# Kernel optimization log

Measured on AMD Instinct MI355X. Metric: run time of the kernel, lower is better.

## Reference

```python
import jax, jax.numpy as jnp
import numpy as np
from jax import lax

N, CIN, H, W = 128, 1024, 14, 14
CF, TH = 128, 128          # cv_filter, te_hidden
HP, GT, FP, A = 256, 256, 256, 32


def setup_inputs() -> dict:
    key = jax.random.key(0)
    ks = jax.random.split(key, 12)
    s = 0.05
    return {
        "image": jax.random.normal(ks[0], (N, CIN, H, W), jnp.float32),
        "code": jax.random.normal(ks[1], (N, TH), jnp.float32),
        "conv_w": jax.random.normal(ks[2], (CF, CIN, 3, 3), jnp.float32) * 0.02,
        "conv_b": jnp.zeros((CF,), jnp.float32),
        "hp_w0": jax.random.normal(ks[3], (CF + 2 + TH, HP), jnp.float32) * s,
        "hp_b0": jnp.zeros((HP,), jnp.float32),
        "hp_w1": jax.random.normal(ks[4], (HP, 1), jnp.float32) * s,
        "hp_b1": jnp.zeros((1,), jnp.float32),
        "gt_w0": jax.random.normal(ks[5], ((CF + 2) * 2 + TH, GT), jnp.float32) * s,
        "gt_b0": jnp.zeros((GT,), jnp.float32),
        "gt_w1": jax.random.normal(ks[6], (GT, GT), jnp.float32) * s,
        "gt_b1": jnp.zeros((GT,), jnp.float32),
        "fp_w0": jax.random.normal(ks[7], (GT, FP), jnp.float32) * s,
        "fp_b0": jnp.zeros((FP,), jnp.float32),
        "fp_w1": jax.random.normal(ks[8], (FP, A), jnp.float32) * s,
        "fp_b1": jnp.zeros((A,), jnp.float32),
    }


def _sarn(image, code, conv_w, conv_b, hp_w0, hp_b0, hp_w1, hp_b1,
          gt_w0, gt_b0, gt_w1, gt_b1, fp_w0, fp_b0, fp_w1, fp_b1):
    # visual_resize: 3x3 conv, stride 1, pad 1 (NCHW)
    x = lax.conv_general_dilated(image, conv_w, (1, 1), "SAME",
                                 dimension_numbers=("NCHW", "OIHW", "NCHW"))
    x = x + conv_b[None, :, None, None]                       # [n, cf, h, w]
    n, c, h, w = x.shape
    o = h * w
    # sarn_encode: append x/y coordinate channels and question code
    xc = jnp.broadcast_to(jnp.linspace(-1.0, 1.0, h).reshape(1, 1, h, 1), (n, 1, h, w))
    yc = jnp.broadcast_to(jnp.linspace(-1.0, 1.0, w).reshape(1, 1, 1, w), (n, 1, h, w))
    coord = jnp.concatenate([x, xc, yc], axis=1)              # [n, cf+2, h, w]
    q = jnp.broadcast_to(code[:, :, None, None], (n, code.shape[1], h, w))
    qenc = jnp.concatenate([coord, q], axis=1)                # [n, cf+2+th, h, w]
    ce = coord.reshape(n, c + 2, o).transpose(0, 2, 1)        # [n, o, cf+2]
    qe = qenc.reshape(n, -1, o).transpose(0, 2, 1)            # [n, o, cf+2+th]
    # h_psi: per-object attention logit
    a = jax.nn.relu(jnp.einsum("nod,dh->noh", qe, hp_w0) + hp_b0)
    att = jnp.einsum("noh,hk->nok", a, hp_w1) + hp_b1         # [n, o, 1]
    # sarn_pair: softmax select a single soft object, pair with every object
    sel = jax.nn.softmax(att[..., 0], axis=1)                 # [n, o]
    selected = jnp.einsum("no,nod->nd", sel, ce)              # [n, cf+2]
    pairs = jnp.concatenate(
        [qe, jnp.broadcast_to(selected[:, None, :], ce.shape)], axis=2)  # [n, o, 2*(cf+2)+th]
    # g_theta MLP + sum over objects
    g = jax.nn.relu(jnp.einsum("nop,pg->nog", pairs, gt_w0) + gt_b0)
    g = jax.nn.relu(jnp.einsum("nog,gk->nok", g, gt_w1) + gt_b1)
    relations = g.sum(axis=1)                                 # [n, gt]
    # f_phi MLP -> answer logits
    f = jax.nn.relu(relations @ fp_w0 + fp_b0)
    return f @ fp_w1 + fp_b1                                  # [n, a_size]


def reference(image, code, conv_w, conv_b, hp_w0, hp_b0, hp_w1, hp_b1,
              gt_w0, gt_b0, gt_w1, gt_b1, fp_w0, fp_b0, fp_w1, fp_b1):
    return _sarn(image, code, conv_w, conv_b, hp_w0, hp_b0, hp_w1, hp_b1,
                 gt_w0, gt_b0, gt_w1, gt_b1, fp_w0, fp_b0, fp_w1, fp_b1)
```

## Files before the change

kernel.cpp:

```cpp
#include <hip/hip_runtime.h>
#include <stdint.h>

typedef unsigned short u16;
typedef __bf16 bf16x8 __attribute__((ext_vector_type(8)));
typedef float f32x4 __attribute__((ext_vector_type(4)));

__device__ __forceinline__ u16 f2b(float f) {
  union { float f; uint32_t u; } v; v.f = f;
  uint32_t r = v.u + 0x7fffu + ((v.u >> 16) & 1u);
  return (u16)(r >> 16);
}
__device__ __forceinline__ float b2f(u16 b) {
  union { float f; uint32_t u; } v; v.u = ((uint32_t)b) << 16;
  return v.f;
}
__device__ __forceinline__ void g2l16(const void* g, void* l) {
  __builtin_amdgcn_global_load_lds(
      (const __attribute__((address_space(1))) void*)g,
      (__attribute__((address_space(3))) void*)l, 16, 0, 0);
}

#define N_SAMP 128
#define OPAD   224
#define ROWS   (N_SAMP * OPAD)
#define KQ     160

#define R_HP   40960
#define R_GT0  40960
#define R_GT1  65536
#define R_BHP  32768
#define R_BGT  32768
#define R_QC   (ROWS * 8)
#define R_QP   114688
#define R_ATT  7168
#define R_REL  8192
#define R_CNT  32
#define R_CVA  917504
__global__ __launch_bounds__(256) void prep_all(
    const float* __restrict__ conv_w, const float* __restrict__ image,
    const float* __restrict__ hp_w0, const float* __restrict__ gt_w0,
    const float* __restrict__ gt_w1, const float* __restrict__ hp_b0,
    const float* __restrict__ gt_b0, const float* __restrict__ code,
    u16* __restrict__ W2, u16* __restrict__ imgT,
    u16* __restrict__ hp_w0t, u16* __restrict__ gt_w0t, u16* __restrict__ gt_w1t,
    float* __restrict__ biasHP, float* __restrict__ biasGT, u16* __restrict__ qeb,
    float* __restrict__ att, float* __restrict__ relations,
    int* __restrict__ doneCnt, float* __restrict__ convAcc) {
  __shared__ float ls[64 * 197];
  int bid = blockIdx.x;
  int t = threadIdx.x;

  if (bid < 512) {
    int p0 = bid << 8;
    const float* src = conv_w + (size_t)p0 * 9;
#pragma unroll
    for (int i = 0; i < 9; ++i) ls[t + i * 256] = src[t + i * 256];
    __syncthreads();
#pragma unroll
    for (int s = 0; s < 9; ++s)
      W2[s * 131072 + p0 + t] = f2b(ls[t * 9 + s]);
    return;
  }
  bid -= 512;

  if (bid < 2048) {
    float (*tt)[197] = (float(*)[197])ls;
    int n = bid >> 4;
    int cin0 = (bid & 15) * 64;
    const float* src = image + ((size_t)n * 1024 + cin0) * 196;
    for (int e = t; e < 64 * 196; e += 256) {
      int c = e / 196, sp = e % 196;
      tt[c][sp] = src[c * 196 + sp];
    }
    __syncthreads();
#pragma unroll
    for (int i = 0; i < 8; ++i) {
      int qid = t + i * 256;
      int spg = qid >> 3, qd = qid & 7;
      int gy = spg >> 4, gx = spg & 15;
      uint4 pk = {0u, 0u, 0u, 0u};
      if (gy >= 1 && gy <= 14 && gx >= 1 && gx <= 14) {
        int sp = (gy - 1) * 14 + (gx - 1);
        uint32_t vv[8];
#pragma unroll
        for (int j = 0; j < 8; ++j) vv[j] = f2b(tt[qd * 8 + j][sp]);
        pk.x = vv[0] | (vv[1] << 16);
        pk.y = vv[2] | (vv[3] << 16);
        pk.z = vv[4] | (vv[5] << 16);
        pk.w = vv[6] | (vv[7] << 16);
      }
      *(uint4*)(imgT + (((size_t)(n * 256 + spg)) << 10) + cin0 + qd * 8) = pk;
    }
    return;
  }
  bid -= 2048;

  int idx = bid * 256 + t;
  if (idx < R_HP) {
    int nn = idx / KQ, kk = idx % KQ;
    hp_w0t[idx] = (kk < 130) ? f2b(hp_w0[kk * 256 + nn]) : (u16)0;
    return;
  }
  idx -= R_HP;
  if (idx < R_GT0) {
    int nn = idx / KQ, kk = idx % KQ;
    gt_w0t[idx] = (kk < 130) ? f2b(gt_w0[kk * 256 + nn]) : (u16)0;
    return;
  }
  idx -= R_GT0;
  if (idx < R_GT1) {
    int nn = idx >> 8, kk = idx & 255;
    gt_w1t[idx] = f2b(gt_w1[kk * 256 + nn]);
    return;
  }
  idx -= R_GT1;
  if (idx < R_BHP) {
    int n = idx >> 8, tc = idx & 255;
    float acc = hp_b0[tc];
    for (int d = 0; d < 128; ++d) acc += code[n * 128 + d] * hp_w0[(130 + d) * 256 + tc];
    biasHP[idx] = acc;
    return;
  }
  idx -= R_BHP;
  if (idx < R_BGT) {
    int n = idx >> 8, tc = idx & 255;
    float acc = gt_b0[tc];
    for (int d = 0; d < 128; ++d) acc += code[n * 128 + d] * gt_w0[(130 + d) * 256 + tc];
    biasGT[idx] = acc;
    return;
  }
  idx -= R_BGT;
  if (idx < R_QC) {
    int row = idx >> 3, qd = idx & 7;
    int o = row % 224;
    ushort4 v = {0, 0, 0, 0};
    if (o < 196 && qd == 0) {
      int y = o / 14, x = o % 14;
      v.x = f2b(-1.f + 2.f * y / 13.f);
      v.y = f2b(-1.f + 2.f * x / 13.f);
    }
    *(ushort4*)(qeb + (size_t)row * KQ + 128 + qd * 4) = v;
    return;
  }
  idx -= R_QC;
  if (idx < R_QP) {
    int pr = idx >> 5, qd = idx & 31;
    int row = (pr / 28) * 224 + 196 + (pr % 28);
    *(ushort4*)(qeb + (size_t)row * KQ + qd * 4) = (ushort4){0, 0, 0, 0};
    return;
  }
  idx -= R_QP;
  if (idx < R_ATT) { *((float4*)att + idx) = (float4){0.f, 0.f, 0.f, 0.f}; return; }
  idx -= R_ATT;
  if (idx < R_REL) { *((float4*)relations + idx) = (float4){0.f, 0.f, 0.f, 0.f}; return; }
  idx -= R_REL;
  if (idx < R_CNT) { *((float4*)doneCnt + idx) = (float4){0.f, 0.f, 0.f, 0.f}; return; }
  idx -= R_CNT;
  if (idx < R_CVA) *((float4*)convAcc + idx) = (float4){0.f, 0.f, 0.f, 0.f};
}

__global__ __launch_bounds__(256) void conv_gemm(
    const u16* __restrict__ imgT, const u16* __restrict__ W2,
    float* __restrict__ convAcc) {
  __shared__ __align__(16) u16 lA[112 * 64];
  __shared__ __align__(16) u16 lB[128 * 64];
  int tid = threadIdx.x, lane = tid & 63, w = tid >> 6;
  int wg = blockIdx.x;
  int xcd = wg & 7, grp = wg >> 3;
  int n = ((grp / 6) << 3) | xcd;
  int r6 = grp % 6;
  int oh = r6 / 3, ks = r6 % 3;
  int oBase = oh * 112;
  size_t nBase = (size_t)n << 8;
  int rowIn = lane >> 3;
  int cA = ((lane & 7) ^ rowIn) << 3;

  int yxA[4];
  for (int ii = 0; ii < 4; ++ii) {
    int t = w + ii * 4;
    int o = oBase + t * 8 + rowIn;
    bool valid = o < 196;
    int y = o / 14, x = o - y * 14;
    yxA[ii] = valid ? (y * 16 + x) : 0;
  }

  f32x4 acc[7][2];
#pragma unroll
  for (int mt = 0; mt < 7; ++mt)
#pragma unroll
    for (int j = 0; j < 2; ++j) acc[mt][j] = (f32x4){0.f, 0.f, 0.f, 0.f};

  int l = lane & 15, q = lane >> 4;
  for (int si = 0; si < 3; ++si) {
    int s = ks * 3 + si;
    int off = (s / 3) * 16 + (s % 3);
    const u16* Ws = W2 + ((size_t)(s * 128) << 10);
    for (int cb = 0; cb < 16; ++cb) {
      int k0 = cb << 6;
      __syncthreads();
      g2l16(imgT + ((nBase + (size_t)(yxA[0] + off)) << 10) + k0 + cA, &lA[(w) * 512]);
      g2l16(imgT + ((nBase + (size_t)(yxA[1] + off)) << 10) + k0 + cA, &lA[(w + 4) * 512]);
      g2l16(imgT + ((nBase + (size_t)(yxA[2] + off)) << 10) + k0 + cA, &lA[(w + 8) * 512]);
      if (w < 2)
        g2l16(imgT + ((nBase + (size_t)(yxA[3] + off)) << 10) + k0 + cA, &lA[(w + 12) * 512]);
#pragma unroll
      for (int ii = 0; ii < 4; ++ii) {
        int t = w + ii * 4;
        g2l16(Ws + ((size_t)(t * 8 + rowIn) << 10) + k0 + cA, &lB[t * 512]);
      }
      __syncthreads();
#pragma unroll
      for (int kk = 0; kk < 2; ++kk) {
        int co = ((((kk << 2) | q) ^ (l & 7)) << 3);
        bf16x8 af[7];
#pragma unroll
        for (int mt = 0; mt < 7; ++mt)
          af[mt] = *(const bf16x8*)&lA[(mt * 16 + l) * 64 + co];
#pragma unroll
        for (int jj = 0; jj < 2; ++jj) {
          bf16x8 bb = *(const bf16x8*)&lB[(w * 32 + jj * 16 + l) * 64 + co];
#pragma unroll
          for (int mt = 0; mt < 7; ++mt)
            acc[mt][jj] = __builtin_amdgcn_mfma_f32_16x16x32_bf16(af[mt], bb, acc[mt][jj], 0, 0, 0);
        }
      }
    }
  }
#pragma unroll
  for (int mt = 0; mt < 7; ++mt) {
    int o = oBase + mt * 16 + q * 4;
#pragma unroll
    for (int r4 = 0; r4 < 4; ++r4) {
      if (o + r4 < 196) {
        float* dst = convAcc + (size_t)(n * 224 + o + r4) * 128 + w * 32 + l;
        atomicAdd(dst, acc[mt][0][r4]);
        atomicAdd(dst + 16, acc[mt][1][r4]);
      }
    }
  }
}

__global__ __launch_bounds__(256) void conv_fix(
    const float* __restrict__ convAcc, const float* __restrict__ conv_b,
    u16* __restrict__ qeb) {
  int idx = blockIdx.x * 256 + threadIdx.x;
  int row196 = idx >> 5;
  int c0 = (idx & 31) << 2;
  int n = row196 / 196, o = row196 - n * 196;
  size_t row = (size_t)(n * 224 + o);
  const float4 v = *(const float4*)(convAcc + (row << 7) + c0);
  const float4 b = *(const float4*)(conv_b + c0);
  ushort4 pk;
  pk.x = f2b(v.x + b.x); pk.y = f2b(v.y + b.y);
  pk.z = f2b(v.z + b.z); pk.w = f2b(v.w + b.w);
  *(ushort4*)(qeb + row * KQ + c0) = pk;
}

template <int MODE, int KP, int KC>
__global__ __launch_bounds__(256) void gemm_kernel(
    const u16* __restrict__ A, const u16* __restrict__ Bt,
    const float* __restrict__ bias, const float* __restrict__ vec,
    float* __restrict__ outF, u16* __restrict__ outB) {
  __shared__ __align__(16) u16 lA[2][128 * 32];
  __shared__ __align__(16) u16 lB[2][128 * 32];
  int tid = threadIdx.x, lane = tid & 63, w = tid >> 6;
  int bx = blockIdx.x, by = blockIdx.y;
  int r0 = bx * 112;
  int cBase = by * 128;
  int kb = (((lane & 3) ^ ((lane >> 3) & 3)) << 3);
  int rA0 = r0 + w * 16 + (lane >> 2);
  int rA1 = r0 + (w + 4) * 16 + (lane >> 2);
  const u16* gA0 = A + (size_t)rA0 * KP + kb;
  const u16* gA1 = A + (size_t)rA1 * KP + kb;
  int cB0 = cBase + w * 16 + (lane >> 2);
  int cB1 = cBase + (w + 4) * 16 + (lane >> 2);
  const u16* gB0 = Bt + (size_t)cB0 * KP + kb;
  const u16* gB1 = Bt + (size_t)cB1 * KP + kb;

  f32x4 acc[7][2];
#pragma unroll
  for (int mt = 0; mt < 7; ++mt)
#pragma unroll
    for (int j = 0; j < 2; ++j) acc[mt][j] = (f32x4){0.f, 0.f, 0.f, 0.f};
  int colW = w * 32;
  int l = lane & 15, q = lane >> 4;
  int co = ((q ^ ((l >> 1) & 3)) << 3);

  auto STAGE = [&](int buf, int cb) {
    g2l16(gA0 + cb * 32, &lA[buf][w * 512]);
    g2l16(gA1 + cb * 32, &lA[buf][(w + 4) * 512]);
    g2l16(gB0 + cb * 32, &lB[buf][w * 512]);
    g2l16(gB1 + cb * 32, &lB[buf][(w + 4) * 512]);
  };

  auto COMPUTE = [&](int cur) {
    bf16x8 af[7];
#pragma unroll
    for (int mt = 0; mt < 7; ++mt)
      af[mt] = *(const bf16x8*)&lA[cur][(mt * 16 + l) * 32 + co];
#pragma unroll
    for (int j = 0; j < 2; ++j) {
      bf16x8 bfr = *(const bf16x8*)&lB[cur][(colW + j * 16 + l) * 32 + co];
#pragma unroll
      for (int mt = 0; mt < 7; ++mt)
        acc[mt][j] = __builtin_amdgcn_mfma_f32_16x16x32_bf16(af[mt], bfr, acc[mt][j], 0, 0, 0);
    }
  };

  STAGE(0, 0);
#pragma unroll
  for (int it = 0; it < KC - 1; ++it) {
    STAGE((it & 1) ^ 1, it + 1);
    asm volatile("s_waitcnt vmcnt(4)" ::: "memory");
    __builtin_amdgcn_s_barrier();
    __builtin_amdgcn_sched_barrier(0);
    COMPUTE(it & 1);
    __builtin_amdgcn_s_barrier();
    __builtin_amdgcn_sched_barrier(0);
  }
  asm volatile("s_waitcnt vmcnt(0)" ::: "memory");
  __builtin_amdgcn_s_barrier();
  __builtin_amdgcn_sched_barrier(0);
  COMPUTE((KC - 1) & 1);

  int q4 = lane >> 4, c = lane & 15;
  {
    int n = bx >> 1;
    float attp[7][4];
#pragma unroll
    for (int mt = 0; mt < 7; ++mt)
#pragma unroll
      for (int r = 0; r < 4; ++r) attp[mt][r] = 0.f;
#pragma unroll
    for (int j = 0; j < 2; ++j) {
      int col = cBase + colW + j * 16 + c;
      float b0 = bias[n * 256 + col], w1 = vec[col];
#pragma unroll
      for (int mt = 0; mt < 7; ++mt)
#pragma unroll
        for (int r = 0; r < 4; ++r) {
          float v = fmaxf(acc[mt][j][r] + b0, 0.f);
          attp[mt][r] += v * w1;
        }
    }
#pragma unroll
    for (int mt = 0; mt < 7; ++mt)
#pragma unroll
      for (int r = 0; r < 4; ++r) {
        float p = attp[mt][r];
        p += __shfl_xor(p, 1, 64);
        p += __shfl_xor(p, 2, 64);
        p += __shfl_xor(p, 4, 64);
        p += __shfl_xor(p, 8, 64);
        if (c == 0) atomicAdd(&outF[r0 + mt * 16 + q4 * 4 + r], p);
      }
  }
}

__global__ __launch_bounds__(256) void sel_kernel(
    const float* __restrict__ att, const u16* __restrict__ qeb,
    const float* __restrict__ gt_w0, const float* __restrict__ biasGT,
    float* __restrict__ bias2) {
  int n = blockIdx.x, t = threadIdx.x;
  int w = t >> 6, lane = t & 63;
  __shared__ u16 sq[196][130];
  __shared__ float sm[196];
  __shared__ float sel[130];
  __shared__ float red[8];
  const u16* base = qeb + (size_t)n * 224 * KQ;
  for (int o = w; o < 196; o += 4) {
    const u16* rowp = base + (size_t)o * KQ;
    for (int c = lane; c < 130; c += 64) sq[o][c] = rowp[c];
  }
  float a = (t < 196) ? att[n * 224 + t] : -1e30f;
  float m = a;
  for (int mask = 1; mask < 64; mask <<= 1) m = fmaxf(m, __shfl_xor(m, mask, 64));
  if (lane == 0) red[w] = m;
  __syncthreads();
  float M = fmaxf(fmaxf(red[0], red[1]), fmaxf(red[2], red[3]));
  float e = (t < 196) ? expf(a - M) : 0.f;
  float sAcc = e;
  for (int mask = 1; mask < 64; mask <<= 1) sAcc += __shfl_xor(sAcc, mask, 64);
  if (lane == 0) red[4 + w] = sAcc;
  __syncthreads();
  float S = red[4] + red[5] + red[6] + red[7];
  if (t < 196) sm[t] = e / S;
  __syncthreads();
  if (t < 130) {
    float acc = 0.f;
    for (int o = 0; o < 196; ++o) acc += sm[o] * b2f(sq[o][t]);
    sel[t] = acc;
  }
  __syncthreads();
  float acc2 = biasGT[n * 256 + t];
  for (int d = 0; d < 130; ++d) acc2 += sel[d] * gt_w0[(258 + d) * 256 + t];
  bias2[n * 256 + t] = acc2;
}

__global__ __launch_bounds__(256) void g_fused(
    const u16* __restrict__ qeb, const u16* __restrict__ gt_w0t,
    const u16* __restrict__ gt_w1t, const float* __restrict__ bias2,
    const float* __restrict__ gt_b1, const float* __restrict__ fp_w0,
    const float* __restrict__ fp_b0, const float* __restrict__ fp_w1,
    const float* __restrict__ fp_b1, float* __restrict__ relations,
    int* __restrict__ doneCnt, float* __restrict__ out) {
  __shared__ __align__(16) u16 panel[112 * 256];
  __shared__ __align__(16) u16 lA[2][128 * 32];
  __shared__ __align__(16) u16 lB[2][256 * 32];
  __shared__ int flag;
  int tid = threadIdx.x, lane = tid & 63, w = tid >> 6;
  int bx = blockIdx.x;
  int n = bx >> 1;
  int r0 = bx * 112;
  int kb = (((lane & 3) ^ ((lane >> 3) & 3)) << 3);
  int rowIn = lane >> 2;
  const u16* gA0 = qeb + (size_t)(r0 + w * 16 + rowIn) * KQ + kb;
  const u16* gA1 = qeb + (size_t)(r0 + (w + 4) * 16 + rowIn) * KQ + kb;
  int l = lane & 15, q = lane >> 4;
  int co = ((q ^ ((l >> 1) & 3)) << 3);

  f32x4 acc[7][4];
#pragma unroll
  for (int mt = 0; mt < 7; ++mt)
#pragma unroll
    for (int j = 0; j < 4; ++j) acc[mt][j] = (f32x4){0.f, 0.f, 0.f, 0.f};

  auto STAGE1 = [&](int buf, int cb) {
    g2l16(gA0 + cb * 32, &lA[buf][w * 512]);
    g2l16(gA1 + cb * 32, &lA[buf][(w + 4) * 512]);
#pragma unroll
    for (int ii = 0; ii < 4; ++ii) {
      int t = w + ii * 4;
      g2l16(gt_w0t + (size_t)(t * 16 + rowIn) * KQ + kb + cb * 32, &lB[buf][t * 512]);
    }
  };
  auto COMPUTE1 = [&](int cur) {
    bf16x8 af[7];
#pragma unroll
    for (int mt = 0; mt < 7; ++mt)
      af[mt] = *(const bf16x8*)&lA[cur][(mt * 16 + l) * 32 + co];
#pragma unroll
    for (int j = 0; j < 4; ++j) {
      bf16x8 bfr = *(const bf16x8*)&lB[cur][(w * 64 + j * 16 + l) * 32 + co];
#pragma unroll
      for (int mt = 0; mt < 7; ++mt)
        acc[mt][j] = __builtin_amdgcn_mfma_f32_16x16x32_bf16(af[mt], bfr, acc[mt][j], 0, 0, 0);
    }
  };

  STAGE1(0, 0);
#pragma unroll
  for (int it = 0; it < 4; ++it) {
    STAGE1((it + 1) & 1, it + 1);
    asm volatile("s_waitcnt vmcnt(6)" ::: "memory");
    __builtin_amdgcn_s_barrier();
    __builtin_amdgcn_sched_barrier(0);
    COMPUTE1(it & 1);
    __builtin_amdgcn_s_barrier();
    __builtin_amdgcn_sched_barrier(0);
  }
  asm volatile("s_waitcnt vmcnt(0)" ::: "memory");
  __builtin_amdgcn_s_barrier();
  __builtin_amdgcn_sched_barrier(0);
  COMPUTE1(0);

  auto STAGE2 = [&](int buf, int kb2) {
#pragma unroll
    for (int ii = 0; ii < 4; ++ii) {
      int t = w + ii * 4;
      g2l16(gt_w1t + (size_t)(t * 16 + rowIn) * 256 + kb + kb2 * 32, &lB[buf][t * 512]);
    }
  };
  STAGE2(1, 0);

#pragma unroll
  for (int j = 0; j < 4; ++j) {
    int col = w * 64 + j * 16 + l;
    float b = bias2[n * 256 + col];
    int chA = col >> 3, inA = col & 7;
#pragma unroll
    for (int mt = 0; mt < 7; ++mt)
#pragma unroll
      for (int r = 0; r < 4; ++r) {
        int row = mt * 16 + q * 4 + r;
        float v = fmaxf(acc[mt][j][r] + b, 0.f);
        panel[row * 256 + ((chA ^ (row & 7)) << 3) + inA] = f2b(v);
      }
  }
  __syncthreads();

  f32x4 acc2[7][4];
#pragma unroll
  for (int mt = 0; mt < 7; ++mt)
#pragma unroll
    for (int j = 0; j < 4; ++j) acc2[mt][j] = (f32x4){0.f, 0.f, 0.f, 0.f};

#pragma unroll
  for (int kb2 = 0; kb2 < 8; ++kb2) {
    if (kb2 < 7) {
      STAGE2(kb2 & 1, kb2 + 1);
      asm volatile("s_waitcnt vmcnt(4)" ::: "memory");
    } else {
      asm volatile("s_waitcnt vmcnt(0)" ::: "memory");
    }
    __builtin_amdgcn_s_barrier();
    __builtin_amdgcn_sched_barrier(0);
    int cur = 1 - (kb2 & 1);
    bf16x8 af[7];
#pragma unroll
    for (int mt = 0; mt < 7; ++mt) {
      int row = mt * 16 + l;
      int ch = (kb2 * 4 + q) ^ (row & 7);
      af[mt] = *(const bf16x8*)&panel[row * 256 + (ch << 3)];
    }
#pragma unroll
    for (int j = 0; j < 4; ++j) {
      bf16x8 bfr = *(const bf16x8*)&lB[cur][(w * 64 + j * 16 + l) * 32 + co];
#pragma unroll
      for (int mt = 0; mt < 7; ++mt)
        acc2[mt][j] = __builtin_amdgcn_mfma_f32_16x16x32_bf16(af[mt], bfr, acc2[mt][j], 0, 0, 0);
    }
    __builtin_amdgcn_s_barrier();
    __builtin_amdgcn_sched_barrier(0);
  }

  int ob = (bx & 1) * 112;
#pragma unroll
  for (int j = 0; j < 4; ++j) {
    int col = w * 64 + j * 16 + l;
    float b = gt_b1[col];
    float sum = 0.f;
#pragma unroll
    for (int mt = 0; mt < 7; ++mt)
#pragma unroll
      for (int r = 0; r < 4; ++r) {
        int o = ob + mt * 16 + q * 4 + r;
        if (o < 196) sum += fmaxf(acc2[mt][j][r] + b, 0.f);
      }
    sum += __shfl_xor(sum, 16, 64);
    sum += __shfl_xor(sum, 32, 64);
    if (q == 0) atomicAdd(&relations[n * 256 + col], sum);
  }

  __threadfence();
  if (tid == 0) flag = atomicAdd(&doneCnt[n], 1);
  __syncthreads();
  if (flag == 1) {
    float* rel = (float*)panel;
    float* f = rel + 256;
    rel[tid] = atomicAdd(&relations[n * 256 + tid], 0.0f);
    __syncthreads();
    float acc3 = fp_b0[tid];
    for (int k = 0; k < 256; ++k) acc3 += rel[k] * fp_w0[k * 256 + tid];
    f[tid] = fmaxf(acc3, 0.f);
    __syncthreads();
    if (tid < 32) {
      float o = fp_b1[0];
      for (int k = 0; k < 256; ++k) o += f[k] * fp_w1[k * 32 + tid];
      out[n * 32 + tid] = o;
    }
  }
}

extern "C" void kernel_launch(void* const* d_in, const int* in_sizes, int n_in,
                              void* d_out, int out_size, void* d_ws, size_t ws_size,
                              hipStream_t stream) {
  const float* image = (const float*)d_in[0];
  const float* code = (const float*)d_in[1];
  const float* conv_w = (const float*)d_in[2];
  const float* conv_b = (const float*)d_in[3];
  const float* hp_w0 = (const float*)d_in[4];
  const float* hp_b0 = (const float*)d_in[5];
  const float* hp_w1 = (const float*)d_in[6];
  const float* gt_w0 = (const float*)d_in[8];
  const float* gt_b0 = (const float*)d_in[9];
  const float* gt_w1 = (const float*)d_in[10];
  const float* gt_b1 = (const float*)d_in[11];
  const float* fp_w0 = (const float*)d_in[12];
  const float* fp_b0 = (const float*)d_in[13];
  const float* fp_w1 = (const float*)d_in[14];
  const float* fp_b1 = (const float*)d_in[15];
  float* out = (float*)d_out;

  char* p = (char*)d_ws;
  u16* imgT = (u16*)p;   p += (size_t)128 * 256 * 1024 * 2;
  u16* W2 = (u16*)p;     p += (size_t)9 * 128 * 1024 * 2;
  u16* qeb = (u16*)p;    p += (size_t)ROWS * KQ * 2;
  u16* hp_w0t = (u16*)p; p += (size_t)256 * KQ * 2;
  u16* gt_w0t = (u16*)p; p += (size_t)256 * KQ * 2;
  u16* gt_w1t = (u16*)p; p += (size_t)256 * 256 * 2;
  float* att = (float*)p;    p += (size_t)ROWS * 4;
  float* bias2 = (float*)p;  p += (size_t)128 * 256 * 4;
  float* biasHP = (float*)p; p += (size_t)128 * 256 * 4;
  float* biasGT = (float*)p; p += (size_t)128 * 256 * 4;
  float* convAcc = (float*)p; p += (size_t)ROWS * 128 * 4;
  float* relations = (float*)p; p += (size_t)128 * 256 * 4;
  int* doneCnt = (int*)p; p += 512;

  prep_all<<<8381, 256, 0, stream>>>(conv_w, image, hp_w0, gt_w0, gt_w1, hp_b0, gt_b0,
                                     code, W2, imgT, hp_w0t, gt_w0t, gt_w1t,
                                     biasHP, biasGT, qeb, att, relations, doneCnt, convAcc);
  conv_gemm<<<768, 256, 0, stream>>>(imgT, W2, convAcc);
  conv_fix<<<3136, 256, 0, stream>>>(convAcc, conv_b, qeb);
  gemm_kernel<0, KQ, 5><<<dim3(256, 2), 256, 0, stream>>>(qeb, hp_w0t, biasHP, hp_w1, att, nullptr);
  sel_kernel<<<128, 256, 0, stream>>>(att, qeb, gt_w0, biasGT, bias2);
  g_fused<<<256, 256, 0, stream>>>(qeb, gt_w0t, gt_w1t, bias2, gt_b1,
                                   fp_w0, fp_b0, fp_w1, fp_b1, relations, doneCnt, out);
}
```

Before: 369.2 us.

## Fuse softmax-select into attention GEMM and split g_theta into two GEMM kernels

The softmax/select step now runs in the last-arriving block of the attention GEMM, found with a per-sample atomic counter, so the separate sel_kernel launch goes away. The fused g_theta kernel, which used 256 blocks with a 256-column panel, is split into two 512-block GEMMs. The intermediate activation goes through global memory in the reused convAcc buffer, and the f_phi tail runs in the last block of the second GEMM. This doubles grid parallelism for the g_theta stage, at the cost of an extra global write and read of the hidden activation plus one more kernel launch.

```diff
diff --git a/kernel.cpp b/kernel.cpp
--- a/kernel.cpp
+++ b/kernel.cpp
@@ -34,7 +34,7 @@
 #define R_QP   114688
 #define R_ATT  7168
 #define R_REL  8192
-#define R_CNT  32
+#define R_CNT  64
 #define R_CVA  917504
 __global__ __launch_bounds__(256) void prep_all(
     const float* __restrict__ conv_w, const float* __restrict__ image,
@@ -45,7 +45,7 @@
     u16* __restrict__ hp_w0t, u16* __restrict__ gt_w0t, u16* __restrict__ gt_w1t,
     float* __restrict__ biasHP, float* __restrict__ biasGT, u16* __restrict__ qeb,
     float* __restrict__ att, float* __restrict__ relations,
-    int* __restrict__ doneCnt, float* __restrict__ convAcc) {
+    int* __restrict__ cnts, float* __restrict__ convAcc) {
   __shared__ float ls[64 * 197];
   int bid = blockIdx.x;
   int t = threadIdx.x;
@@ -154,7 +154,7 @@
   idx -= R_ATT;
   if (idx < R_REL) { *((float4*)relations + idx) = (float4){0.f, 0.f, 0.f, 0.f}; return; }
   idx -= R_REL;
-  if (idx < R_CNT) { *((float4*)doneCnt + idx) = (float4){0.f, 0.f, 0.f, 0.f}; return; }
+  if (idx < R_CNT) { *((float4*)cnts + idx) = (float4){0.f, 0.f, 0.f, 0.f}; return; }
   idx -= R_CNT;
   if (idx < R_CVA) *((float4*)convAcc + idx) = (float4){0.f, 0.f, 0.f, 0.f};
 }
@@ -256,26 +256,29 @@
   *(ushort4*)(qeb + row * KQ + c0) = pk;
 }
 
-template <int MODE, int KP, int KC>
-__global__ __launch_bounds__(256) void gemm_kernel(
+__global__ __launch_bounds__(256) void gemm0_sel(
     const u16* __restrict__ A, const u16* __restrict__ Bt,
-    const float* __restrict__ bias, const float* __restrict__ vec,
-    float* __restrict__ outF, u16* __restrict__ outB) {
-  __shared__ __align__(16) u16 lA[2][128 * 32];
-  __shared__ __align__(16) u16 lB[2][128 * 32];
+    const float* __restrict__ biasHP, const float* __restrict__ hp_w1,
+    float* __restrict__ att, const u16* __restrict__ qeb,
+    const float* __restrict__ gt_w0, const float* __restrict__ biasGT,
+    float* __restrict__ bias2, int* __restrict__ selCnt) {
+  union __align__(16) SM0 {
+    struct { u16 lA[2][4096]; u16 lB[2][4096]; } g;
+    struct { u16 sq[196][130]; float smx[196]; float sel[130]; float red[8]; } s;
+  };
+  __shared__ SM0 S;
+  __shared__ int sflag;
+  const int KP = KQ, KC = 5;
   int tid = threadIdx.x, lane = tid & 63, w = tid >> 6;
   int bx = blockIdx.x, by = blockIdx.y;
   int r0 = bx * 112;
   int cBase = by * 128;
+  int n = bx >> 1;
   int kb = (((lane & 3) ^ ((lane >> 3) & 3)) << 3);
-  int rA0 = r0 + w * 16 + (lane >> 2);
-  int rA1 = r0 + (w + 4) * 16 + (lane >> 2);
-  const u16* gA0 = A + (size_t)rA0 * KP + kb;
-  const u16* gA1 = A + (size_t)rA1 * KP + kb;
-  int cB0 = cBase + w * 16 + (lane >> 2);
-  int cB1 = cBase + (w + 4) * 16 + (lane >> 2);
-  const u16* gB0 = Bt + (size_t)cB0 * KP + kb;
-  const u16* gB1 = Bt + (size_t)cB1 * KP + kb;
+  const u16* gA0 = A + (size_t)(r0 + w * 16 + (lane >> 2)) * KP + kb;
+  const u16* gA1 = A + (size_t)(r0 + (w + 4) * 16 + (lane >> 2)) * KP + kb;
+  const u16* gB0 = Bt + (size_t)(cBase + w * 16 + (lane >> 2)) * KP + kb;
+  const u16* gB1 = Bt + (size_t)(cBase + (w + 4) * 16 + (lane >> 2)) * KP + kb;
 
   f32x4 acc[7][2];
 #pragma unroll
@@ -287,20 +290,19 @@
   int co = ((q ^ ((l >> 1) & 3)) << 3);
 
   auto STAGE = [&](int buf, int cb) {
-    g2l16(gA0 + cb * 32, &lA[buf][w * 512]);
-    g2l16(gA1 + cb * 32, &lA[buf][(w + 4) * 512]);
-    g2l16(gB0 + cb * 32, &lB[buf][w * 512]);
-    g2l16(gB1 + cb * 32, &lB[buf][(w + 4) * 512]);
+    g2l16(gA0 + cb * 32, &S.g.lA[buf][w * 512]);
+    g2l16(gA1 + cb * 32, &S.g.lA[buf][(w + 4) * 512]);
+    g2l16(gB0 + cb * 32, &S.g.lB[buf][w * 512]);
+    g2l16(gB1 + cb * 32, &S.g.lB[buf][(w + 4) * 512]);
   };
-
   auto COMPUTE = [&](int cur) {
     bf16x8 af[7];
 #pragma unroll
     for (int mt = 0; mt < 7; ++mt)
-      af[mt] = *(const bf16x8*)&lA[cur][(mt * 16 + l) * 32 + co];
+      af[mt] = *(const bf16x8*)&S.g.lA[cur][(mt * 16 + l) * 32 + co];
 #pragma unroll
     for (int j = 0; j < 2; ++j) {
-      bf16x8 bfr = *(const bf16x8*)&lB[cur][(colW + j * 16 + l) * 32 + co];
+      bf16x8 bfr = *(const bf16x8*)&S.g.lB[cur][(colW + j * 16 + l) * 32 + co];
 #pragma unroll
       for (int mt = 0; mt < 7; ++mt)
         acc[mt][j] = __builtin_amdgcn_mfma_f32_16x16x32_bf16(af[mt], bfr, acc[mt][j], 0, 0, 0);
@@ -325,7 +327,6 @@
 
   int q4 = lane >> 4, c = lane & 15;
   {
-    int n = bx >> 1;
     float attp[7][4];
 #pragma unroll
     for (int mt = 0; mt < 7; ++mt)
@@ -334,7 +335,7 @@
 #pragma unroll
     for (int j = 0; j < 2; ++j) {
       int col = cBase + colW + j * 16 + c;
-      float b0 = bias[n * 256 + col], w1 = vec[col];
+      float b0 = biasHP[n * 256 + col], w1 = hp_w1[col];
 #pragma unroll
       for (int mt = 0; mt < 7; ++mt)
 #pragma unroll
@@ -352,213 +353,224 @@
         p += __shfl_xor(p, 2, 64);
         p += __shfl_xor(p, 4, 64);
         p += __shfl_xor(p, 8, 64);
-        if (c == 0) atomicAdd(&outF[r0 + mt * 16 + q4 * 4 + r], p);
+        if (c == 0) atomicAdd(&att[r0 + mt * 16 + q4 * 4 + r], p);
       }
   }
-}
-
-__global__ __launch_bounds__(256) void sel_kernel(
-    const float* __restrict__ att, const u16* __restrict__ qeb,
-    const float* __restrict__ gt_w0, const float* __restrict__ biasGT,
-    float* __restrict__ bias2) {
-  int n = blockIdx.x, t = threadIdx.x;
-  int w = t >> 6, lane = t & 63;
-  __shared__ u16 sq[196][130];
-  __shared__ float sm[196];
-  __shared__ float sel[130];
-  __shared__ float red[8];
+
+  __threadfence();
+  if (tid == 0) sflag = atomicAdd(&selCnt[n], 1);
+  __syncthreads();
+  if (sflag != 3) return;
+
+  int t = tid;
   const u16* base = qeb + (size_t)n * 224 * KQ;
   for (int o = w; o < 196; o += 4) {
     const u16* rowp = base + (size_t)o * KQ;
-    for (int c = lane; c < 130; c += 64) sq[o][c] = rowp[c];
-  }
-  float a = (t < 196) ? att[n * 224 + t] : -1e30f;
+    for (int cc = lane; cc < 130; cc += 64) S.s.sq[o][cc] = rowp[cc];
+  }
+  float a = (t < 196) ? atomicAdd(&att[n * 224 + t], 0.0f) : -1e30f;
   float m = a;
   for (int mask = 1; mask < 64; mask <<= 1) m = fmaxf(m, __shfl_xor(m, mask, 64));
-  if (lane == 0) red[w] = m;
-  __syncthreads();
-  float M = fmaxf(fmaxf(red[0], red[1]), fmaxf(red[2], red[3]));
+  if (lane == 0) S.s.red[w] = m;
+  __syncthreads();
+  float M = fmaxf(fmaxf(S.s.red[0], S.s.red[1]), fmaxf(S.s.red[2], S.s.red[3]));
   float e = (t < 196) ? expf(a - M) : 0.f;
   float sAcc = e;
   for (int mask = 1; mask < 64; mask <<= 1) sAcc += __shfl_xor(sAcc, mask, 64);
-  if (lane == 0) red[4 + w] = sAcc;
-  __syncthreads();
-  float S = red[4] + red[5] + red[6] + red[7];
-  if (t < 196) sm[t] = e / S;
+  if (lane == 0) S.s.red[4 + w] = sAcc;
+  __syncthreads();
+  float Ssum = S.s.red[4] + S.s.red[5] + S.s.red[6] + S.s.red[7];
+  if (t < 196) S.s.smx[t] = e / Ssum;
   __syncthreads();
   if (t < 130) {
-    float acc = 0.f;
-    for (int o = 0; o < 196; ++o) acc += sm[o] * b2f(sq[o][t]);
-    sel[t] = acc;
+    float acc2 = 0.f;
+    for (int o = 0; o < 196; ++o) acc2 += S.s.smx[o] * b2f(S.s.sq[o][t]);
+    S.s.sel[t] = acc2;
   }
   __syncthreads();
   float acc2 = biasGT[n * 256 + t];
-  for (int d = 0; d < 130; ++d) acc2 += sel[d] * gt_w0[(258 + d) * 256 + t];
+  for (int d = 0; d < 130; ++d) acc2 += S.s.sel[d] * gt_w0[(258 + d) * 256 + t];
   bias2[n * 256 + t] = acc2;
 }
 
-__global__ __launch_bounds__(256) void g_fused(
-    const u16* __restrict__ qeb, const u16* __restrict__ gt_w0t,
-    const u16* __restrict__ gt_w1t, const float* __restrict__ bias2,
-    const float* __restrict__ gt_b1, const float* __restrict__ fp_w0,
-    const float* __restrict__ fp_b0, const float* __restrict__ fp_w1,
-    const float* __restrict__ fp_b1, float* __restrict__ relations,
-    int* __restrict__ doneCnt, float* __restrict__ out) {
-  __shared__ __align__(16) u16 panel[112 * 256];
+__global__ __launch_bounds__(256) void gemm1_k(
+    const u16* __restrict__ A, const u16* __restrict__ Bt,
+    const float* __restrict__ bias2, u16* __restrict__ outB) {
   __shared__ __align__(16) u16 lA[2][128 * 32];
-  __shared__ __align__(16) u16 lB[2][256 * 32];
-  __shared__ int flag;
+  __shared__ __align__(16) u16 lB[2][128 * 32];
+  const int KP = KQ, KC = 5;
   int tid = threadIdx.x, lane = tid & 63, w = tid >> 6;
-  int bx = blockIdx.x;
-  int n = bx >> 1;
+  int bx = blockIdx.x, by = blockIdx.y;
   int r0 = bx * 112;
+  int cBase = by * 128;
   int kb = (((lane & 3) ^ ((lane >> 3) & 3)) << 3);
-  int rowIn = lane >> 2;
-  const u16* gA0 = qeb + (size_t)(r0 + w * 16 + rowIn) * KQ + kb;
-  const u16* gA1 = qeb + (size_t)(r0 + (w + 4) * 16 + rowIn) * KQ + kb;
+  const u16* gA0 = A + (size_t)(r0 + w * 16 + (lane >> 2)) * KP + kb;
+  const u16* gA1 = A + (size_t)(r0 + (w + 4) * 16 + (lane >> 2)) * KP + kb;
+  const u16* gB0 = Bt + (size_t)(cBase + w * 16 + (lane >> 2)) * KP + kb;
+  const u16* gB1 = Bt + (size_t)(cBase + (w + 4) * 16 + (lane >> 2)) * KP + kb;
+
+  f32x4 acc[7][2];
+#pragma unroll
+  for (int mt = 0; mt < 7; ++mt)
+#pragma unroll
+    for (int j = 0; j < 2; ++j) acc[mt][j] = (f32x4){0.f, 0.f, 0.f, 0.f};
+  int colW = w * 32;
   int l = lane & 15, q = lane >> 4;
   int co = ((q ^ ((l >> 1) & 3)) << 3);
 
-  f32x4 acc[7][4];
-#pragma unroll
-  for (int mt = 0; mt < 7; ++mt)
-#pragma unroll
-    for (int j = 0; j < 4; ++j) acc[mt][j] = (f32x4){0.f, 0.f, 0.f, 0.f};
-
-  auto STAGE1 = [&](int buf, int cb) {
+  auto STAGE = [&](int buf, int cb) {
     g2l16(gA0 + cb * 32, &lA[buf][w * 512]);
     g2l16(gA1 + cb * 32, &lA[buf][(w + 4) * 512]);
-#pragma unroll
-    for (int ii = 0; ii < 4; ++ii) {
-      int t = w + ii * 4;
-      g2l16(gt_w0t + (size_t)(t * 16 + rowIn) * KQ + kb + cb * 32, &lB[buf][t * 512]);
-    }
+    g2l16(gB0 + cb * 32, &lB[buf][w * 512]);
+    g2l16(gB1 + cb * 32, &lB[buf][(w + 4) * 512]);
   };
-  auto COMPUTE1 = [&](int cur) {
+  auto COMPUTE = [&](int cur) {
     bf16x8 af[7];
 #pragma unroll
     for (int mt = 0; mt < 7; ++mt)
       af[mt] = *(const bf16x8*)&lA[cur][(mt * 16 + l) * 32 + co];
 #pragma unroll
-    for (int j = 0; j < 4; ++j) {
-      bf16x8 bfr = *(const bf16x8*)&lB[cur][(w * 64 + j * 16 + l) * 32 + co];
+    for (int j = 0; j < 2; ++j) {
+      bf16x8 bfr = *(const bf16x8*)&lB[cur][(colW + j * 16 + l) * 32 + co];
 #pragma unroll
       for (int mt = 0; mt < 7; ++mt)
         acc[mt][j] = __builtin_amdgcn_mfma_f32_16x16x32_bf16(af[mt], bfr, acc[mt][j], 0, 0, 0);
     }
   };
 
-  STAGE1(0, 0);
-#pragma unroll
-  for (int it = 0; it < 4; ++it) {
-    STAGE1((it + 1) & 1, it + 1);
-    asm volatile("s_waitcnt vmcnt(6)" ::: "memory");
+  STAGE(0, 0);
+#pragma unroll
+  for (int it = 0; it < KC - 1; ++it) {
+    STAGE((it & 1) ^ 1, it + 1);
+    asm volatile("s_waitcnt vmcnt(4)" ::: "memory");
     __builtin_amdgcn_s_barrier();
     __builtin_amdgcn_sched_barrier(0);
-    COMPUTE1(it & 1);
+    COMPUTE(it & 1);
     __builtin_amdgcn_s_barrier();
     __builtin_amdgcn_sched_barrier(0);
   }
   asm volatile("s_waitcnt vmcnt(0)" ::: "memory");
   __builtin_amdgcn_s_barrier();
   __builtin_amdgcn_sched_barrier(0);
-  COMPUTE1(0);
-
-  auto STAGE2 = [&](int buf, int kb2) {
-#pragma unroll
-    for (int ii = 0; ii < 4; ++ii) {
-      int t = w + ii * 4;
-      g2l16(gt_w1t + (size_t)(t * 16 + rowIn) * 256 + kb + kb2 * 32, &lB[buf][t * 512]);
-    }
+  COMPUTE((KC - 1) & 1);
+
+  int q4 = lane >> 4, c = lane & 15;
+  int n = bx >> 1;
+#pragma unroll
+  for (int mt = 0; mt < 7; ++mt)
+#pragma unroll
+    for (int j = 0; j < 2; ++j) {
+      int col = cBase + colW + j * 16 + c;
+      float b = bias2[n * 256 + col];
+#pragma unroll
+      for (int r = 0; r < 4; ++r) {
+        int row = r0 + mt * 16 + q4 * 4 + r;
+        outB[(size_t)row * 256 + col] = f2b(fmaxf(acc[mt][j][r] + b, 0.f));
+      }
+    }
+}
+
+__global__ __launch_bounds__(256) void gemm2_fphi(
+    const u16* __restrict__ A, const u16* __restrict__ Bt,
+    const float* __restrict__ gt_b1, float* __restrict__ relations,
+    const float* __restrict__ fp_w0, const float* __restrict__ fp_b0,
+    const float* __restrict__ fp_w1, const float* __restrict__ fp_b1,
+    float* __restrict__ out, int* __restrict__ relCnt) {
+  __shared__ __align__(16) u16 lA[2][128 * 32];
+  __shared__ __align__(16) u16 lB[2][128 * 32];
+  __shared__ int rflag;
+  const int KP = 256, KC = 8;
+  int tid = threadIdx.x, lane = tid & 63, w = tid >> 6;
+  int bx = blockIdx.x, by = blockIdx.y;
+  int r0 = bx * 112;
+  int cBase = by * 128;
+  int n = bx >> 1;
+  int kb = (((lane & 3) ^ ((lane >> 3) & 3)) << 3);
+  const u16* gA0 = A + (size_t)(r0 + w * 16 + (lane >> 2)) * KP + kb;
+  const u16* gA1 = A + (size_t)(r0 + (w + 4) * 16 + (lane >> 2)) * KP + kb;
+  const u16* gB0 = Bt + (size_t)(cBase + w * 16 + (lane >> 2)) * KP + kb;
+  const u16* gB1 = Bt + (size_t)(cBase + (w + 4) * 16 + (lane >> 2)) * KP + kb;
+
+  f32x4 acc[7][2];
+#pragma unroll
+  for (int mt = 0; mt < 7; ++mt)
+#pragma unroll
+    for (int j = 0; j < 2; ++j) acc[mt][j] = (f32x4){0.f, 0.f, 0.f, 0.f};
+  int colW = w * 32;
+  int l = lane & 15, q = lane >> 4;
+  int co = ((q ^ ((l >> 1) & 3)) << 3);
+
+  auto STAGE = [&](int buf, int cb) {
+    g2l16(gA0 + cb * 32, &lA[buf][w * 512]);
+    g2l16(gA1 + cb * 32, &lA[buf][(w + 4) * 512]);
+    g2l16(gB0 + cb * 32, &lB[buf][w * 512]);
+    g2l16(gB1 + cb * 32, &lB[buf][(w + 4) * 512]);
   };
-  STAGE2(1, 0);
-
-#pragma unroll
-  for (int j = 0; j < 4; ++j) {
-    int col = w * 64 + j * 16 + l;
-    float b = bias2[n * 256 + col];
-    int chA = col >> 3, inA = col & 7;
+  auto COMPUTE = [&](int cur) {
+    bf16x8 af[7];
 #pragma unroll
     for (int mt = 0; mt < 7; ++mt)
-#pragma unroll
-      for (int r = 0; r < 4; ++r) {
-        int row = mt * 16 + q * 4 + r;
-        float v = fmaxf(acc[mt][j][r] + b, 0.f);
-        panel[row * 256 + ((chA ^ (row & 7)) << 3) + inA] = f2b(v);
-      }
-  }
-  __syncthreads();
-
-  f32x4 acc2[7][4];
-#pragma unroll
-  for (int mt = 0; mt < 7; ++mt)
-#pragma unroll
-    for (int j = 0; j < 4; ++j) acc2[mt][j] = (f32x4){0.f, 0.f, 0.f, 0.f};
-
-#pragma unroll
-  for (int kb2 = 0; kb2 < 8; ++kb2) {
-    if (kb2 < 7) {
-      STAGE2(kb2 & 1, kb2 + 1);
-      asm volatile("s_waitcnt vmcnt(4)" ::: "memory");
-    } else {
-      asm volatile("s_waitcnt vmcnt(0)" ::: "memory");
-    }
+      af[mt] = *(const bf16x8*)&lA[cur][(mt * 16 + l) * 32 + co];
+#pragma unroll
+    for (int j = 0; j < 2; ++j) {
+      bf16x8 bfr = *(const bf16x8*)&lB[cur][(colW + j * 16 + l) * 32 + co];
+#pragma unroll
+      for (int mt = 0; mt < 7; ++mt)
+        acc[mt][j] = __builtin_amdgcn_mfma_f32_16x16x32_bf16(af[mt], bfr, acc[mt][j], 0, 0, 0);
+    }
+  };
+
+  STAGE(0, 0);
+#pragma unroll
+  for (int it = 0; it < KC - 1; ++it) {
+    STAGE((it & 1) ^ 1, it + 1);
+    asm volatile("s_waitcnt vmcnt(4)" ::: "memory");
     __builtin_amdgcn_s_barrier();
     __builtin_amdgcn_sched_barrier(0);
-    int cur = 1 - (kb2 & 1);
-    bf16x8 af[7];
-#pragma unroll
-    for (int mt = 0; mt < 7; ++mt) {
-      int row = mt * 16 + l;
-      int ch = (kb2 * 4 + q) ^ (row & 7);
-      af[mt] = *(const bf16x8*)&panel[row * 256 + (ch << 3)];
-    }
-#pragma unroll
-    for (int j = 0; j < 4; ++j) {
-      bf16x8 bfr = *(const bf16x8*)&lB[cur][(w * 64 + j * 16 + l) * 32 + co];
-#pragma unroll
-      for (int mt = 0; mt < 7; ++mt)
-        acc2[mt][j] = __builtin_amdgcn_mfma_f32_16x16x32_bf16(af[mt], bfr, acc2[mt][j], 0, 0, 0);
-    }
+    COMPUTE(it & 1);
     __builtin_amdgcn_s_barrier();
     __builtin_amdgcn_sched_barrier(0);
   }
-
+  asm volatile("s_waitcnt vmcnt(0)" ::: "memory");
+  __builtin_amdgcn_s_barrier();
+  __builtin_amdgcn_sched_barrier(0);
+  COMPUTE((KC - 1) & 1);
+
+  int q4 = lane >> 4, c = lane & 15;
   int ob = (bx & 1) * 112;
 #pragma unroll
-  for (int j = 0; j < 4; ++j) {
-    int col = w * 64 + j * 16 + l;
+  for (int j = 0; j < 2; ++j) {
+    int col = cBase + colW + j * 16 + c;
     float b = gt_b1[col];
     float sum = 0.f;
 #pragma unroll
     for (int mt = 0; mt < 7; ++mt)
 #pragma unroll
       for (int r = 0; r < 4; ++r) {
-        int o = ob + mt * 16 + q * 4 + r;
-        if (o < 196) sum += fmaxf(acc2[mt][j][r] + b, 0.f);
+        int o = ob + mt * 16 + q4 * 4 + r;
+        if (o < 196) sum += fmaxf(acc[mt][j][r] + b, 0.f);
       }
     sum += __shfl_xor(sum, 16, 64);
     sum += __shfl_xor(sum, 32, 64);
-    if (q == 0) atomicAdd(&relations[n * 256 + col], sum);
+    if (q4 == 0) atomicAdd(&relations[n * 256 + col], sum);
   }
 
   __threadfence();
-  if (tid == 0) flag = atomicAdd(&doneCnt[n], 1);
-  __syncthreads();
-  if (flag == 1) {
-    float* rel = (float*)panel;
-    float* f = rel + 256;
-    rel[tid] = atomicAdd(&relations[n * 256 + tid], 0.0f);
-    __syncthreads();
-    float acc3 = fp_b0[tid];
-    for (int k = 0; k < 256; ++k) acc3 += rel[k] * fp_w0[k * 256 + tid];
-    f[tid] = fmaxf(acc3, 0.f);
-    __syncthreads();
-    if (tid < 32) {
-      float o = fp_b1[0];
-      for (int k = 0; k < 256; ++k) o += f[k] * fp_w1[k * 32 + tid];
-      out[n * 32 + tid] = o;
-    }
+  if (tid == 0) rflag = atomicAdd(&relCnt[n], 1);
+  __syncthreads();
+  if (rflag != 3) return;
+  float* rel = (float*)lA;
+  float* f = rel + 256;
+  rel[tid] = atomicAdd(&relations[n * 256 + tid], 0.0f);
+  __syncthreads();
+  float acc3 = fp_b0[tid];
+  for (int k = 0; k < 256; ++k) acc3 += rel[k] * fp_w0[k * 256 + tid];
+  f[tid] = fmaxf(acc3, 0.f);
+  __syncthreads();
+  if (tid < 32) {
+    float o = fp_b1[0];
+    for (int k = 0; k < 256; ++k) o += f[k] * fp_w1[k * 32 + tid];
+    out[n * 32 + tid] = o;
   }
 }
 
@@ -595,15 +607,19 @@
   float* biasGT = (float*)p; p += (size_t)128 * 256 * 4;
   float* convAcc = (float*)p; p += (size_t)ROWS * 128 * 4;
   float* relations = (float*)p; p += (size_t)128 * 256 * 4;
-  int* doneCnt = (int*)p; p += 512;
+  int* cnts = (int*)p; p += 1024;
+  int* selCnt = cnts;
+  int* relCnt = cnts + 128;
+  u16* g1 = (u16*)convAcc;
 
   prep_all<<<8381, 256, 0, stream>>>(conv_w, image, hp_w0, gt_w0, gt_w1, hp_b0, gt_b0,
                                      code, W2, imgT, hp_w0t, gt_w0t, gt_w1t,
-                                     biasHP, biasGT, qeb, att, relations, doneCnt, convAcc);
+                                     biasHP, biasGT, qeb, att, relations, cnts, convAcc);
   conv_gemm<<<768, 256, 0, stream>>>(imgT, W2, convAcc);
   conv_fix<<<3136, 256, 0, stream>>>(convAcc, conv_b, qeb);
-  gemm_kernel<0, KQ, 5><<<dim3(256, 2), 256, 0, stream>>>(qeb, hp_w0t, biasHP, hp_w1, att, nullptr);
-  sel_kernel<<<128, 256, 0, stream>>>(att, qeb, gt_w0, biasGT, bias2);
-  g_fused<<<256, 256, 0, stream>>>(qeb, gt_w0t, gt_w1t, bias2, gt_b1,
-                                   fp_w0, fp_b0, fp_w1, fp_b1, relations, doneCnt, out);
-}
+  gemm0_sel<<<dim3(256, 2), 256, 0, stream>>>(qeb, hp_w0t, biasHP, hp_w1, att,
+                                              qeb, gt_w0, biasGT, bias2, selCnt);
+  gemm1_k<<<dim3(256, 2), 256, 0, stream>>>(qeb, gt_w0t, bias2, g1);
+  gemm2_fphi<<<dim3(256, 2), 256, 0, stream>>>(g1, gt_w1t, gt_b1, relations,
+                                               fp_w0, fp_b0, fp_w1, fp_b1, out, relCnt);
+}
```

New measurement: 412.7 us. 11.8% more time.
